# Performance work log

Measured on AMD Instinct MI355X. Metric: run time of the kernel, lower is better.

Reference implementation:

```python
import jax, jax.numpy as jnp
import numpy as np

D_MODEL = 2048
D_INNER = 2048
N_QK = 32
N_V = 32
D_STATE = 64
D_CONV = 4
CHUNK = 128
CONV_DIM = D_INNER + 2 * N_QK * D_STATE  # 6144
IN_OUT = 2 * D_INNER + 2 * N_QK * D_STATE + N_V  # 8224


def setup_inputs() -> dict:
    key = jax.random.key(0)
    ks = jax.random.split(key, 6)
    u = jax.random.normal(ks[0], (2, 4096, D_MODEL), dtype=jnp.float32)
    W_in = jax.random.normal(ks[1], (IN_OUT, D_MODEL), dtype=jnp.float32) * 0.02
    conv_w = jax.random.normal(ks[2], (CONV_DIM, D_CONV), dtype=jnp.float32) * 0.2
    conv_b = jax.random.normal(ks[3], (CONV_DIM,), dtype=jnp.float32) * 0.02
    D = jnp.ones((N_V,), dtype=jnp.float32)
    z_bias = jnp.zeros((D_INNER,), dtype=jnp.float32)
    W_out = jax.random.normal(ks[4], (D_MODEL, D_INNER), dtype=jnp.float32) * 0.02
    return {"u": u, "W_in": W_in, "conv_w": conv_w, "conv_b": conv_b,
            "D": D, "z_bias": z_bias, "W_out": W_out}


def causal_depthwise_conv(x, w, b):
    # x: [B, L, C]; w: [C, K]; b: [C]. Torch Conv1d(groups=C, padding=K-1)[..., :L]
    B, L, C = x.shape
    K = w.shape[1]
    xp = jnp.pad(x, ((0, 0), (K - 1, 0), (0, 0)))
    y = b[None, None, :]
    for k in range(K):
        y = y + xp[:, k:k + L, :] * w[None, None, :, k]
    return y


def ssd_chunk_scan(x, dt, B, C, chunk):
    # Mamba2 SSD with A = -1 per head.
    # x: [b,l,h,p], dt: [b,l,h] (positive), B,C: [b,l,h,n]
    b, l, h, p = x.shape
    n = B.shape[-1]
    nc = l // chunk
    x = x.reshape(b, nc, chunk, h, p)
    dt = dt.reshape(b, nc, chunk, h)
    B = B.reshape(b, nc, chunk, h, n)
    C = C.reshape(b, nc, chunk, h, n)
    a = -dt                                  # A * dt
    cum = jnp.cumsum(a, axis=2)              # [b,nc,q,h]
    xdt = x * dt[..., None]                  # dt_t * x_t
    # ---- intra-chunk (causal, decay exp(cum_q - cum_k), q >= k) ----
    CB = jnp.einsum('bcqhn,bckhn->bchqk', C, B)
    cumT = jnp.swapaxes(cum, 2, 3)           # [b,nc,h,q]
    diff = cumT[..., :, None] - cumT[..., None, :]   # [b,nc,h,q,k]
    mask = jnp.tril(jnp.ones((chunk, chunk), dtype=bool))
    decay = jnp.exp(jnp.where(mask, diff, -jnp.inf))
    y_intra = jnp.einsum('bchqk,bckhp->bcqhp', CB * decay, xdt)
    # ---- per-chunk final states ----
    state_decay = jnp.exp(cum[:, :, -1:, :] - cum)   # [b,nc,q,h]
    states = jnp.einsum('bckhn,bckhp->bchpn', B * state_decay[..., None], xdt)
    chunk_decay = jnp.exp(cum[:, :, -1, :])          # [b,nc,h]
    # ---- inter-chunk recurrence ----
    def step(carry, inp):
        st, cd = inp  # st [b,h,p,n], cd [b,h]
        new = carry * cd[:, :, None, None] + st
        return new, carry  # emit the state *entering* this chunk
    init = jnp.zeros((b, h, p, n), dtype=x.dtype)
    _, prev = jax.lax.scan(step, init,
                           (jnp.moveaxis(states, 1, 0), jnp.moveaxis(chunk_decay, 1, 0)))
    prev = jnp.moveaxis(prev, 0, 1)                  # [b,nc,h,p,n]
    y_inter = jnp.einsum('bcqhn,bchpn->bcqhp', C * jnp.exp(cum)[..., None], prev)
    return (y_intra + y_inter).reshape(b, l, h, p)


def reference(u, W_in, conv_w, conv_b, D, z_bias, W_out):
    b, l, _ = u.shape  # l divisible by CHUNK (padded_len == l)
    xBCzA = jnp.einsum('bld,od->blo', u, W_in)
    xBC = xBCzA[..., :CONV_DIM]
    z = xBCzA[..., CONV_DIM:CONV_DIM + D_INNER]
    A_log = xBCzA[..., CONV_DIM + D_INNER:]
    xBC = causal_depthwise_conv(xBC, conv_w, conv_b)  # activation = identity
    x = xBC[..., :D_INNER]
    Bm = xBC[..., D_INNER:D_INNER + N_QK * D_STATE]
    Cm = xBC[..., D_INNER + N_QK * D_STATE:]
    x = x.reshape(b, l, N_V, D_INNER // N_V)
    Bm = Bm.reshape(b, l, N_QK, D_STATE)
    Cm = Cm.reshape(b, l, N_QK, D_STATE)
    dt = jax.nn.softplus(A_log)                       # [b,l,h]
    x_scan = x / dt[..., None]
    y = ssd_chunk_scan(x_scan, dt, Bm, Cm, CHUNK)
    y = y + D[None, None, :, None] * x                # Du uses undivided x
    y = y.reshape(b, l, D_INNER)
    out = jnp.einsum('bli,oi->blo', y * jax.nn.silu(z + z_bias), W_out)
    return out
```

## Files before the change

kernel.cpp:

```cpp
#include <hip/hip_runtime.h>
#include <math.h>

#define D_MODEL  2048
#define D_INNER  2048
#define N_QK     32
#define N_V      32
#define D_STATE  64
#define D_CONV   4
#define CHUNK    128
#define CONV_DIM 6144
#define IN_OUT   8224
#define BATCH    2
#define SEQ      4096
#define M_ROWS   (BATCH*SEQ)
#define NCHUNK   (SEQ/CHUNK)

typedef unsigned short bf16_t;
typedef __attribute__((ext_vector_type(4))) float f32x4;
typedef __attribute__((ext_vector_type(8))) short bf16x8;

#define SWZ64(r,c)  ((((r)*64)  + (c)) ^ (((r)&7)<<3))
#define SWZ128(r,c) ((((r)*128) + (c)) ^ (((r)&7)<<3))

__device__ __forceinline__ float b2f(bf16_t u) {
    union { unsigned int i; float f; } w; w.i = ((unsigned int)u) << 16; return w.f;
}
__device__ __forceinline__ bf16_t f2b(float f) {
    unsigned int x = __float_as_uint(f);
    return (bf16_t)((x + 0x7FFFu + ((x >> 16) & 1u)) >> 16);
}
__device__ __forceinline__ void store4b(bf16_t* dst, float4 v) {
    ushort4 u; u.x = f2b(v.x); u.y = f2b(v.y); u.z = f2b(v.z); u.w = f2b(v.w);
    *reinterpret_cast<ushort4*>(dst) = u;
}

__device__ __forceinline__ void gload_lds16(const bf16_t* g, bf16_t* l) {
    __builtin_amdgcn_global_load_lds((const __attribute__((address_space(1))) void*)g,
                                     (__attribute__((address_space(3))) void*)l,
                                     16, 0, 0);
}

__global__ __launch_bounds__(256) void f2b3_kernel(const float* __restrict__ a0, bf16_t* __restrict__ o0, long n0,
                                                   const float* __restrict__ a1, bf16_t* __restrict__ o1, long n1,
                                                   const float* __restrict__ a2, bf16_t* __restrict__ o2, long n2)
{
    const long total = (n0 + n1 + n2) >> 2;
    for (long s = (long)blockIdx.x * 256 + threadIdx.x; s < total; s += (long)gridDim.x * 256) {
        long i = s << 2;
        const float* in; bf16_t* out;
        if (i < n0)           { in = a0 + i; out = o0 + i; }
        else if (i < n0 + n1) { i -= n0; in = a1 + i; out = o1 + i; }
        else                  { i -= n0 + n1; in = a2 + i; out = o2 + i; }
        float4 v = *reinterpret_cast<const float4*>(in);
        ushort4 o;
        o.x = f2b(v.x); o.y = f2b(v.y); o.z = f2b(v.z); o.w = f2b(v.w);
        *reinterpret_cast<ushort4*>(out) = o;
    }
}

template<int NTB, int K, bool OBF16>
__global__ __launch_bounds__(512, 2) void gemm256(const bf16_t* __restrict__ A,
                                                  const bf16_t* __restrict__ B,
                                                  void* __restrict__ Cv,
                                                  long ldc)
{
    constexpr int BK = 64;
    constexpr int NT = K / BK;
    __shared__ bf16_t As[2][2][8192];
    __shared__ bf16_t Bs[2][2][8192];

    const int nwg = gridDim.x;
    const int bid = blockIdx.x;
    const int wg  = ((nwg & 7) == 0) ? ((bid & 7) * (nwg >> 3) + (bid >> 3)) : bid;
    const int bm = (wg / NTB) * 256;
    const int bn = (wg % NTB) * 256;

    const int tid  = threadIdx.x;
    const int lane = tid & 63;
    const int wv   = tid >> 6;
    const int wr   = wv >> 2, wc = wv & 3;
    const int l15  = lane & 15, l4 = lane >> 4;

    f32x4 acc[8][4];
    #pragma unroll
    for (int i = 0; i < 8; ++i)
        #pragma unroll
        for (int j = 0; j < 4; ++j) acc[i][j] = (f32x4){0.f, 0.f, 0.f, 0.f};

    const bf16_t* Abase = A + (long)bm * K;
    const bf16_t* Bbase = B + (long)bn * K;

    auto stage_half = [&](int t, int buf, int kh) {
        #pragma unroll
        for (int it = 0; it < 2; ++it) {
            const int s   = it * 512 + tid;
            const int row = s >> 2;
            const int jp  = s & 3;
            const int jl  = jp ^ ((row >> 1) & 3);
            const long go = (long)row * K + t * BK + kh * 32 + jl * 8;
            gload_lds16(Abase + go, &As[buf][kh][s * 8]);
            gload_lds16(Bbase + go, &Bs[buf][kh][s * 8]);
        }
    };
    auto rdA = [&](int buf, int kh, int row) {
        const int jp = l4 ^ ((row >> 1) & 3);
        return *reinterpret_cast<const bf16x8*>(&As[buf][kh][(row * 4 + jp) * 8]);
    };
    auto rdB = [&](int buf, int kh, int row) {
        const int jp = l4 ^ ((row >> 1) & 3);
        return *reinterpret_cast<const bf16x8*>(&Bs[buf][kh][(row * 4 + jp) * 8]);
    };

    stage_half(0, 0, 0);
    stage_half(0, 0, 1);
    asm volatile("s_waitcnt vmcnt(4)" ::: "memory");
    __builtin_amdgcn_s_barrier();

    for (int t = 0; t < NT; ++t) {
        const int cur = t & 1;
        bf16x8 bfr[4], af[4];
        if (t + 1 < NT) stage_half(t + 1, cur ^ 1, 0);
        #pragma unroll
        for (int ni = 0; ni < 4; ++ni) bfr[ni] = rdB(cur, 0, wc * 64 + ni * 16 + l15);
        #pragma unroll
        for (int mi = 0; mi < 4; ++mi) af[mi] = rdA(cur, 0, wr * 128 + mi * 16 + l15);
        __builtin_amdgcn_s_setprio(1);
        #pragma unroll
        for (int mi = 0; mi < 4; ++mi)
            #pragma unroll
            for (int ni = 0; ni < 4; ++ni)
                acc[mi][ni] = __builtin_amdgcn_mfma_f32_16x16x32_bf16(
                    af[mi], bfr[ni], acc[mi][ni], 0, 0, 0);
        __builtin_amdgcn_s_setprio(0);
        #pragma unroll
        for (int mi = 0; mi < 4; ++mi) af[mi] = rdA(cur, 0, wr * 128 + 64 + mi * 16 + l15);
        __builtin_amdgcn_s_setprio(1);
        #pragma unroll
        for (int mi = 0; mi < 4; ++mi)
            #pragma unroll
            for (int ni = 0; ni < 4; ++ni)
                acc[4 + mi][ni] = __builtin_amdgcn_mfma_f32_16x16x32_bf16(
                    af[mi], bfr[ni], acc[4 + mi][ni], 0, 0, 0);
        __builtin_amdgcn_s_setprio(0);
        if (t + 1 < NT) {
            stage_half(t + 1, cur ^ 1, 1);
            asm volatile("s_waitcnt vmcnt(8)" ::: "memory");
        } else {
            asm volatile("s_waitcnt vmcnt(0)" ::: "memory");
        }
        __builtin_amdgcn_s_barrier();
        #pragma unroll
        for (int ni = 0; ni < 4; ++ni) bfr[ni] = rdB(cur, 1, wc * 64 + ni * 16 + l15);
        #pragma unroll
        for (int mi = 0; mi < 4; ++mi) af[mi] = rdA(cur, 1, wr * 128 + mi * 16 + l15);
        __builtin_amdgcn_s_setprio(1);
        #pragma unroll
        for (int mi = 0; mi < 4; ++mi)
            #pragma unroll
            for (int ni = 0; ni < 4; ++ni)
                acc[mi][ni] = __builtin_amdgcn_mfma_f32_16x16x32_bf16(
                    af[mi], bfr[ni], acc[mi][ni], 0, 0, 0);
        __builtin_amdgcn_s_setprio(0);
        #pragma unroll
        for (int mi = 0; mi < 4; ++mi) af[mi] = rdA(cur, 1, wr * 128 + 64 + mi * 16 + l15);
        __builtin_amdgcn_s_setprio(1);
        #pragma unroll
        for (int mi = 0; mi < 4; ++mi)
            #pragma unroll
            for (int ni = 0; ni < 4; ++ni)
                acc[4 + mi][ni] = __builtin_amdgcn_mfma_f32_16x16x32_bf16(
                    af[mi], bfr[ni], acc[4 + mi][ni], 0, 0, 0);
        __builtin_amdgcn_s_setprio(0);
        if (t + 1 < NT) { asm volatile("s_waitcnt vmcnt(4)" ::: "memory"); }
        __builtin_amdgcn_s_barrier();
    }

    #pragma unroll
    for (int mf = 0; mf < 8; ++mf) {
        const long grow0 = bm + wr * 128 + mf * 16 + l4 * 4;
        #pragma unroll
        for (int ni = 0; ni < 4; ++ni) {
            const int gcol = bn + wc * 64 + ni * 16 + l15;
            #pragma unroll
            for (int j = 0; j < 4; ++j) {
                if (OBF16)
                    ((bf16_t*)Cv)[(grow0 + j) * ldc + gcol] = f2b(acc[mf][ni][j]);
                else
                    ((float*)Cv)[(grow0 + j) * ldc + gcol] = acc[mf][ni][j];
            }
        }
    }
}

template<int N, int K, bool OBF16>
__global__ __launch_bounds__(256) void gemm_mfma(const bf16_t* __restrict__ A,
                                                 const bf16_t* __restrict__ B,
                                                 void* __restrict__ Cv,
                                                 long ldc)
{
    constexpr int BM = 128, BN = 128, BK = 64;
    constexpr int NTB = (N + BN - 1) / BN;
    __shared__ bf16_t As[BM * BK];
    __shared__ bf16_t Bs[BM * BK];

    const int nwg = gridDim.x;
    const int bid = blockIdx.x;
    const int wg  = ((nwg & 7) == 0) ? ((bid & 7) * (nwg >> 3) + (bid >> 3)) : bid;
    const int bm = (wg / NTB) * BM;
    const int bn = (wg % NTB) * BN;

    const int tid  = threadIdx.x;
    const int lane = tid & 63;
    const int wv   = tid >> 6;
    const int wr   = wv >> 1, wc = wv & 1;

    f32x4 acc[4][4];
    #pragma unroll
    for (int i = 0; i < 4; ++i)
        #pragma unroll
        for (int j = 0; j < 4; ++j) acc[i][j] = (f32x4){0.f, 0.f, 0.f, 0.f};

    for (int k0 = 0; k0 < K; k0 += BK) {
        #pragma unroll
        for (int it = 0; it < 4; ++it) {
            const int seg = it * 256 + tid;
            const int row = seg >> 3, c16 = seg & 7;
            gload_lds16(A + (long)(bm + row) * K + k0 + c16 * 8,
                        &As[row * BK + c16 * 8]);
            int brow = bn + row;
            if constexpr (N % BN != 0) brow = min(brow, N - 1);
            gload_lds16(B + (long)brow * K + k0 + c16 * 8,
                        &Bs[row * BK + c16 * 8]);
        }
        __syncthreads();
        #pragma unroll
        for (int kk = 0; kk < 2; ++kk) {
            bf16x8 af[4], bfr[4];
            const int kc = kk * 32 + (lane >> 4) * 8;
            #pragma unroll
            for (int mi = 0; mi < 4; ++mi) {
                const int row = wr * 64 + mi * 16 + (lane & 15);
                af[mi] = *reinterpret_cast<const bf16x8*>(&As[row * BK + kc]);
            }
            #pragma unroll
            for (int ni = 0; ni < 4; ++ni) {
                const int row = wc * 64 + ni * 16 + (lane & 15);
                bfr[ni] = *reinterpret_cast<const bf16x8*>(&Bs[row * BK + kc]);
            }
            #pragma unroll
            for (int mi = 0; mi < 4; ++mi)
                #pragma unroll
                for (int ni = 0; ni < 4; ++ni)
                    acc[mi][ni] = __builtin_amdgcn_mfma_f32_16x16x32_bf16(
                        af[mi], bfr[ni], acc[mi][ni], 0, 0, 0);
        }
        __syncthreads();
    }

    #pragma unroll
    for (int mi = 0; mi < 4; ++mi) {
        const long row0 = bm + wr * 64 + mi * 16 + ((lane >> 4) << 2);
        #pragma unroll
        for (int ni = 0; ni < 4; ++ni) {
            const int col = bn + wc * 64 + ni * 16 + (lane & 15);
            if (N % BN != 0 && col >= N) continue;
            #pragma unroll
            for (int j = 0; j < 4; ++j) {
                if (OBF16)
                    ((bf16_t*)Cv)[(row0 + j) * ldc + col] = f2b(acc[mi][ni][j]);
                else
                    ((float*)Cv)[(row0 + j) * ldc + col] = acc[mi][ni][j];
            }
        }
    }
}

__device__ __forceinline__ float4 conv4v(const bf16_t* __restrict__ xb, long m, int l,
                                         int col, const float* __restrict__ cw,
                                         const float* __restrict__ cbv)
{
    float4 acc = *reinterpret_cast<const float4*>(cbv + col);
    float4 wc0 = *reinterpret_cast<const float4*>(cw + (long)col * 4);
    float4 wc1 = *reinterpret_cast<const float4*>(cw + (long)col * 4 + 4);
    float4 wc2 = *reinterpret_cast<const float4*>(cw + (long)col * 4 + 8);
    float4 wc3 = *reinterpret_cast<const float4*>(cw + (long)col * 4 + 12);
    const float t0[4] = {wc0.x, wc0.y, wc0.z, wc0.w};
    const float t1[4] = {wc1.x, wc1.y, wc1.z, wc1.w};
    const float t2[4] = {wc2.x, wc2.y, wc2.z, wc2.w};
    const float t3[4] = {wc3.x, wc3.y, wc3.z, wc3.w};
    #pragma unroll
    for (int tap = 0; tap < 4; ++tap) {
        if (l - 3 + tap < 0) continue;
        const bf16_t* p = xb + (m - 3 + tap) * (long)IN_OUT + col;
        ushort4 v = *reinterpret_cast<const ushort4*>(p);
        acc.x = fmaf(b2f(v.x), t0[tap], acc.x);
        acc.y = fmaf(b2f(v.y), t1[tap], acc.y);
        acc.z = fmaf(b2f(v.z), t2[tap], acc.z);
        acc.w = fmaf(b2f(v.w), t3[tap], acc.w);
    }
    return acc;
}

template<bool EXP>
__global__ __launch_bounds__(512, 4) void ssd_states(const bf16_t* __restrict__ xb,
                                                     const float* __restrict__ cw,
                                                     const float* __restrict__ cbv,
                                                     bf16_t* __restrict__ states,
                                                     float* __restrict__ cumbuf,
                                                     float* __restrict__ cdecay,
                                                     bf16_t* __restrict__ xtg,
                                                     bf16_t* __restrict__ bg)
{
    const int h = blockIdx.x, c = blockIdx.y, b = blockIdx.z;
    __shared__ bf16_t sx [128 * 64];
    __shared__ bf16_t sBr[128 * 64];
    __shared__ bf16_t sXT[64 * 128];
    __shared__ bf16_t sBT[64 * 128];
    __shared__ float  cum[CHUNK];
    __shared__ float  w0tot;
    const int t = threadIdx.x;
    const long mbase = (long)b * SEQ + (long)c * CHUNK;
    const long cb = ((long)b * NCHUNK + c) * N_QK + h;

    float v = 0.f;
    if (t < CHUNK) {
        const float a = b2f(xb[(mbase + t) * (long)IN_OUT + (CONV_DIM + D_INNER) + h]);
        v = -((a > 20.f) ? a : log1pf(expf(a)));
        #pragma unroll
        for (int s = 1; s < 64; s <<= 1) {
            const float u2 = __shfl_up(v, s, 64);
            if ((t & 63) >= s) v += u2;
        }
        if (t == 63) w0tot = v;
    }
    for (int idx = t; idx < CHUNK * 16; idx += 512) {
        const int k = idx >> 4, q4 = (idx & 15) * 4;
        const long m = mbase + k;
        const int l = (int)(m & (SEQ - 1));
        float4 xv = conv4v(xb, m, l, h * 64 + q4, cw, cbv);
        float4 bv = conv4v(xb, m, l, D_INNER + h * 64 + q4, cw, cbv);
        store4b(&sx [SWZ64(k, q4)], xv);
        store4b(&sBr[SWZ64(k, q4)], bv);
    }
    __syncthreads();
    if (t >= 64 && t < CHUNK) v += w0tot;
    if (t < CHUNK) cum[t] = v;
    __syncthreads();
    const float clast = cum[CHUNK - 1];
    {
        const int j = t & 127;
        const int c8b = (t >> 7) * 2;
        const float ej = __expf(clast - cum[j]);
        #pragma unroll
        for (int it = 0; it < 2; ++it) {
            const int c8 = c8b + it;
            bf16x8 xv = *reinterpret_cast<const bf16x8*>(&sx [SWZ64(j, c8 * 8)]);
            bf16x8 bv = *reinterpret_cast<const bf16x8*>(&sBr[SWZ64(j, c8 * 8)]);
            #pragma unroll
            for (int e = 0; e < 8; ++e) {
                sXT[SWZ128(c8 * 8 + e, j)] = xv[e];
                sBT[SWZ128(c8 * 8 + e, j)] = f2b(b2f((bf16_t)bv[e]) * ej);
            }
        }
    }
    __syncthreads();

    const int lane = t & 63, wv = t >> 6;
    const int l15 = lane & 15, l4 = lane >> 4;
    const int prow  = (wv & 3) * 16;
    const int nbase = (wv >> 2) * 2;
    f32x4 acc[2];
    acc[0] = (f32x4){0.f, 0.f, 0.f, 0.f};
    acc[1] = (f32x4){0.f, 0.f, 0.f, 0.f};
    #pragma unroll
    for (int ks = 0; ks < 4; ++ks) {
        const int kc = ks * 32 + l4 * 8;
        bf16x8 af = *reinterpret_cast<const bf16x8*>(&sXT[SWZ128(prow + l15, kc)]);
        #pragma unroll
        for (int nj = 0; nj < 2; ++nj) {
            bf16x8 bf = *reinterpret_cast<const bf16x8*>(&sBT[SWZ128((nbase + nj) * 16 + l15, kc)]);
            acc[nj] = __builtin_amdgcn_mfma_f32_16x16x32_bf16(af, bf, acc[nj], 0, 0, 0);
        }
    }
    #pragma unroll
    for (int nj = 0; nj < 2; ++nj) {
        #pragma unroll
        for (int jj = 0; jj < 4; ++jj) {
            const int p = prow + l4 * 4 + jj;
            states[cb * 4096 + SWZ64(p, (nbase + nj) * 16 + l15)] = f2b(acc[nj][jj]);
        }
    }
    if constexpr (EXP) {
        #pragma unroll
        for (int it = 0; it < 2; ++it) {
            const int s = it * 512 + t;
            *reinterpret_cast<bf16x8*>(xtg + cb * 8192 + s * 8) =
                *reinterpret_cast<const bf16x8*>(&sXT[s * 8]);
            *reinterpret_cast<bf16x8*>(bg + cb * 8192 + s * 8) =
                *reinterpret_cast<const bf16x8*>(&sBr[s * 8]);
        }
    }
    if (t < CHUNK) cumbuf[cb * CHUNK + t] = cum[t];
    if (t == 0)   cdecay[cb] = __expf(clast);
}

__global__ __launch_bounds__(256) void ssd_scan(bf16_t* __restrict__ states,
                                                const float* __restrict__ cdecay)
{
    const int bid = blockIdx.x;
    const int bh = bid >> 2, q = bid & 3;
    const int b = bh >> 5, h = bh & 31;
    const int t = threadIdx.x;
    __shared__ bf16_t sst[NCHUNK * 1024];
    __shared__ float  scd[NCHUNK];
    if (t < NCHUNK) scd[t] = cdecay[((long)b * NCHUNK + t) * N_QK + h];
    #pragma unroll
    for (int it = 0; it < 16; ++it) {
        const int slot = it * 256 + t;
        const int c = slot >> 7, off = (slot & 127) * 8;
        const long g = (((long)b * NCHUNK + c) * N_QK + h) * 4096 + q * 1024 + off;
        gload_lds16(states + g, &sst[slot * 8]);
    }
    __syncthreads();
    float4 carry = make_float4(0.f, 0.f, 0.f, 0.f);
    for (int c = 0; c < NCHUNK; ++c) {
        ushort4* p = reinterpret_cast<ushort4*>(&sst[c * 1024 + t * 4]);
        const ushort4 su = *p;
        ushort4 pv;
        pv.x = f2b(carry.x); pv.y = f2b(carry.y);
        pv.z = f2b(carry.z); pv.w = f2b(carry.w);
        *p = pv;
        const float cd = scd[c];
        carry.x = fmaf(carry.x, cd, b2f(su.x));
        carry.y = fmaf(carry.y, cd, b2f(su.y));
        carry.z = fmaf(carry.z, cd, b2f(su.z));
        carry.w = fmaf(carry.w, cd, b2f(su.w));
    }
    __syncthreads();
    #pragma unroll
    for (int it = 0; it < 16; ++it) {
        const int slot = it * 256 + t;
        const int c = slot >> 7, off = (slot & 127) * 8;
        const long g = (((long)b * NCHUNK + c) * N_QK + h) * 4096 + q * 1024 + off;
        *reinterpret_cast<bf16x8*>(states + g) =
            *reinterpret_cast<const bf16x8*>(&sst[slot * 8]);
    }
}

template<bool EXP>
__global__ __launch_bounds__(512, 4) void ssd_out(const bf16_t* __restrict__ xb,
                                                  const float* __restrict__ cumbuf,
                                                  const bf16_t* __restrict__ prevst,
                                                  const float* __restrict__ Dvec,
                                                  const float* __restrict__ zbias,
                                                  const float* __restrict__ cw,
                                                  const float* __restrict__ cbv,
                                                  const bf16_t* __restrict__ xtg,
                                                  const bf16_t* __restrict__ bg,
                                                  bf16_t* __restrict__ yz)
{
    const int h = blockIdx.x, c = blockIdx.y, b = blockIdx.z;
    __shared__ bf16_t sC[128 * 64];
    __shared__ bf16_t sB[128 * 64];
    __shared__ bf16_t sXQ[128 * 64];
    __shared__ bf16_t sXT[64 * 128];
    __shared__ bf16_t sP[64 * 64];
    __shared__ float  cum[CHUNK];
    const int t = threadIdx.x;
    const long mbase = (long)b * SEQ + (long)c * CHUNK;
    const long cb = ((long)b * NCHUNK + c) * N_QK + h;
    if (t < CHUNK) cum[t] = cumbuf[cb * CHUNK + t];
    gload_lds16(prevst + cb * 4096 + t * 8, &sP[t * 8]);
    if constexpr (EXP) {
        #pragma unroll
        for (int it = 0; it < 2; ++it) {
            const int s = it * 512 + t;
            gload_lds16(bg  + cb * 8192 + s * 8, &sB [s * 8]);
            gload_lds16(xtg + cb * 8192 + s * 8, &sXT[s * 8]);
        }
        for (int idx = t; idx < CHUNK * 16; idx += 512) {
            const int k = idx >> 4, q4 = (idx & 15) * 4;
            const long m = mbase + k;
            const int l = (int)(m & (SEQ - 1));
            float4 cv = conv4v(xb, m, l, 2 * D_INNER + h * 64 + q4, cw, cbv);
            store4b(&sC[SWZ64(k, q4)], cv);
        }
        __syncthreads();
    } else {
        for (int idx = t; idx < CHUNK * 16; idx += 512) {
            const int k = idx >> 4, q4 = (idx & 15) * 4;
            const long m = mbase + k;
            const int l = (int)(m & (SEQ - 1));
            float4 xv = conv4v(xb, m, l, h * 64 + q4, cw, cbv);
            float4 bv = conv4v(xb, m, l, D_INNER + h * 64 + q4, cw, cbv);
            float4 cv = conv4v(xb, m, l, 2 * D_INNER + h * 64 + q4, cw, cbv);
            store4b(&sXQ[SWZ64(k, q4)], xv);
            store4b(&sB [SWZ64(k, q4)], bv);
            store4b(&sC [SWZ64(k, q4)], cv);
        }
        __syncthreads();
        {
            const int j = t & 127;
            const int c8b = (t >> 7) * 2;
            #pragma unroll
            for (int it = 0; it < 2; ++it) {
                const int c8 = c8b + it;
                bf16x8 v = *reinterpret_cast<const bf16x8*>(&sXQ[SWZ64(j, c8 * 8)]);
                #pragma unroll
                for (int e = 0; e < 8; ++e) sXT[SWZ128(c8 * 8 + e, j)] = v[e];
            }
        }
        __syncthreads();
    }

    const int lane = t & 63, wv = t >> 6;
    const int w16 = wv * 16, l15 = lane & 15, l4 = lane >> 4;
    bf16_t* sQ = sXQ;

    f32x4 yac[4], iac[4];
    #pragma unroll
    for (int np = 0; np < 4; ++np) {
        yac[np] = (f32x4){0.f, 0.f, 0.f, 0.f};
        iac[np] = (f32x4){0.f, 0.f, 0.f, 0.f};
    }

    #pragma unroll
    for (int H = 0; H < 2; ++H) {
        if (H == 1 && wv < 4) break;
        const int j0 = H * 64;
        f32x4 sac[4];
        #pragma unroll
        for (int nj = 0; nj < 4; ++nj) sac[nj] = (f32x4){0.f, 0.f, 0.f, 0.f};
        #pragma unroll
        for (int kk = 0; kk < 2; ++kk) {
            const int kc = kk * 32 + l4 * 8;
            bf16x8 af0 = *reinterpret_cast<const bf16x8*>(&sC[SWZ64(w16 + l15, kc)]);
            #pragma unroll
            for (int nj = 0; nj < 4; ++nj) {
                if (j0 + nj * 16 <= w16 + 15) {
                    bf16x8 bfj = *reinterpret_cast<const bf16x8*>(&sB[SWZ64(j0 + nj * 16 + l15, kc)]);
                    sac[nj] = __builtin_amdgcn_mfma_f32_16x16x32_bf16(af0, bfj, sac[nj], 0, 0, 0);
                }
            }
        }
        #pragma unroll
        for (int nj = 0; nj < 4; ++nj) {
            const int jcol = nj * 16 + l15;
            const int jg = j0 + jcol;
            #pragma unroll
            for (int jj = 0; jj < 4; ++jj) {
                const int i = w16 + l4 * 4 + jj;
                const float q = (jg <= i) ? __expf(cum[i] - cum[jg]) * sac[nj][jj] : 0.f;
                sQ[SWZ64(i, jcol)] = f2b(q);
            }
        }
        #pragma unroll
        for (int kk = 0; kk < 2; ++kk) {
            const int kc = kk * 32 + l4 * 8;
            bf16x8 qa = *reinterpret_cast<const bf16x8*>(&sQ[SWZ64(w16 + l15, kc)]);
            #pragma unroll
            for (int np = 0; np < 4; ++np) {
                bf16x8 xf = *reinterpret_cast<const bf16x8*>(&sXT[SWZ128(np * 16 + l15, j0 + kc)]);
                yac[np] = __builtin_amdgcn_mfma_f32_16x16x32_bf16(qa, xf, yac[np], 0, 0, 0);
            }
        }
    }
    #pragma unroll
    for (int kk = 0; kk < 2; ++kk) {
        const int kc = kk * 32 + l4 * 8;
        bf16x8 cf = *reinterpret_cast<const bf16x8*>(&sC[SWZ64(w16 + l15, kc)]);
        #pragma unroll
        for (int np = 0; np < 4; ++np) {
            bf16x8 pf = *reinterpret_cast<const bf16x8*>(&sP[SWZ64(np * 16 + l15, kc)]);
            iac[np] = __builtin_amdgcn_mfma_f32_16x16x32_bf16(cf, pf, iac[np], 0, 0, 0);
        }
    }
    const float dh = Dvec[h];
    #pragma unroll
    for (int jj = 0; jj < 4; ++jj) {
        const int i = w16 + l4 * 4 + jj;
        const float ei = __expf(cum[i]);
        const long m = mbase + i;
        const bf16_t* zr = xb + m * (long)IN_OUT + CONV_DIM + h * 64;
        bf16_t* orow = yz + m * (long)D_INNER + h * 64;
        #pragma unroll
        for (int np = 0; np < 4; ++np) {
            const int p = np * 16 + l15;
            const float xval = b2f(sXT[SWZ128(p, i)]);
            const float y = yac[np][jj] + ei * iac[np][jj] + dh * xval;
            const float zv = b2f(zr[p]) + zbias[h * 64 + p];
            const float s = zv / (1.f + __expf(-zv));
            orow[p] = f2b(y * s);
        }
    }
}

extern "C" void kernel_launch(void* const* d_in, const int* in_sizes, int n_in,
                              void* d_out, int out_size, void* d_ws, size_t ws_size,
                              hipStream_t stream)
{
    const float* u      = (const float*)d_in[0];
    const float* W_in   = (const float*)d_in[1];
    const float* conv_w = (const float*)d_in[2];
    const float* conv_b = (const float*)d_in[3];
    const float* Dv     = (const float*)d_in[4];
    const float* z_bias = (const float*)d_in[5];
    const float* W_out  = (const float*)d_in[6];
    float* out = (float*)d_out;

    char* w = (char*)d_ws;
    bf16_t* xbcza = (bf16_t*)w;  w += (long)M_ROWS * IN_OUT * 2;
    bf16_t* wob   = (bf16_t*)w;  w += (long)2048 * 2048 * 2;
    char* ureg = w;  w += 67239936;
    bf16_t* ub  = (bf16_t*)ureg;
    bf16_t* wib = (bf16_t*)(ureg + (long)M_ROWS * D_MODEL * 2);
    bf16_t* yzb = (bf16_t*)ureg;
    float*  cumb   = (float*)(ureg + (long)M_ROWS * D_INNER * 2);
    bf16_t* states = (bf16_t*)(cumb + (long)BATCH * NCHUNK * N_QK * CHUNK);
    float*  cdec   = (float*)(states + (long)BATCH * NCHUNK * N_QK * 4096);
    const long base_bytes = (long)(w - (char*)d_ws);
    const long exp_bytes  = 2L * 2048 * 8192 * 2;
    const bool use_exp = ((long)ws_size >= base_bytes + exp_bytes);
    bf16_t* xtg = (bf16_t*)w;
    bf16_t* bg  = xtg + (long)2048 * 8192;

    {
        const long n0 = (long)M_ROWS * D_MODEL;
        const long n1 = (long)IN_OUT * D_MODEL;
        const long n2 = (long)D_MODEL * D_INNER;
        f2b3_kernel<<<2048, 256, 0, stream>>>(u, ub, n0, W_in, wib, n1, W_out, wob, n2);
    }

    gemm256<32, D_MODEL, true><<<(M_ROWS / 256) * 32, 512, 0, stream>>>(
        ub, wib, xbcza, IN_OUT);
    gemm_mfma<32, D_MODEL, true><<<(M_ROWS / 128), 256, 0, stream>>>(
        ub, wib + (long)8192 * D_MODEL, xbcza + 8192, IN_OUT);

    if (use_exp) {
        ssd_states<true><<<dim3(N_QK, NCHUNK, BATCH), 512, 0, stream>>>(
            xbcza, conv_w, conv_b, states, cumb, cdec, xtg, bg);
        ssd_scan<<<BATCH * N_QK * 4, 256, 0, stream>>>(states, cdec);
        ssd_out<true><<<dim3(N_QK, NCHUNK, BATCH), 512, 0, stream>>>(
            xbcza, cumb, states, Dv, z_bias, conv_w, conv_b, xtg, bg, yzb);
    } else {
        ssd_states<false><<<dim3(N_QK, NCHUNK, BATCH), 512, 0, stream>>>(
            xbcza, conv_w, conv_b, states, cumb, cdec, nullptr, nullptr);
        ssd_scan<<<BATCH * N_QK * 4, 256, 0, stream>>>(states, cdec);
        ssd_out<false><<<dim3(N_QK, NCHUNK, BATCH), 512, 0, stream>>>(
            xbcza, cumb, states, Dv, z_bias, conv_w, conv_b, nullptr, nullptr, yzb);
    }

    gemm256<8, D_INNER, false><<<(M_ROWS / 256) * 8, 512, 0, stream>>>(
        yzb, wob, out, D_MODEL);
}
```

Measured before the change: 730.8 us.

## Split-K the narrow A_log projection, precompute softplus dt, widen scan grid

The 32-column A_log projection used to run as a 128x128-tile GEMM on only 64 workgroups, with most of each B tile padding. It is replaced by a split-K kernel over 256 workgroups with a 32-wide B tile and swizzled LDS. A small reduction kernel sums the four partials and applies softplus into an fp32 dt buffer, which ssd_states now reads directly. The chunk-state scan is also split 8 ways per head instead of 4, doubling its grid and halving per-thread work. The cost is one extra launch and extra global traffic for the partial sums, placed in reused workspace.

Result: faster. 713.1 us (-2.4%).

```diff
diff --git a/kernel.cpp b/kernel.cpp
--- a/kernel.cpp
+++ b/kernel.cpp
@@ -192,86 +192,76 @@
     }
 }
 
-template<int N, int K, bool OBF16>
-__global__ __launch_bounds__(256) void gemm_mfma(const bf16_t* __restrict__ A,
-                                                 const bf16_t* __restrict__ B,
-                                                 void* __restrict__ Cv,
-                                                 long ldc)
-{
-    constexpr int BM = 128, BN = 128, BK = 64;
-    constexpr int NTB = (N + BN - 1) / BN;
-    __shared__ bf16_t As[BM * BK];
-    __shared__ bf16_t Bs[BM * BK];
-
-    const int nwg = gridDim.x;
-    const int bid = blockIdx.x;
-    const int wg  = ((nwg & 7) == 0) ? ((bid & 7) * (nwg >> 3) + (bid >> 3)) : bid;
-    const int bm = (wg / NTB) * BM;
-    const int bn = (wg % NTB) * BN;
-
-    const int tid  = threadIdx.x;
-    const int lane = tid & 63;
-    const int wv   = tid >> 6;
-    const int wr   = wv >> 1, wc = wv & 1;
-
-    f32x4 acc[4][4];
-    #pragma unroll
-    for (int i = 0; i < 4; ++i)
-        #pragma unroll
-        for (int j = 0; j < 4; ++j) acc[i][j] = (f32x4){0.f, 0.f, 0.f, 0.f};
-
-    for (int k0 = 0; k0 < K; k0 += BK) {
+__global__ __launch_bounds__(256) void alog_partial(const bf16_t* __restrict__ A,
+                                                    const bf16_t* __restrict__ Bt,
+                                                    float* __restrict__ P)
+{
+    const int rb = blockIdx.x & 63, ks = blockIdx.x >> 6;
+    const int bm = rb * 128;
+    __shared__ bf16_t As[128 * 64];
+    __shared__ bf16_t Bs[32 * 64];
+    const int tid = threadIdx.x, lane = tid & 63, wv = tid >> 6;
+    const int l15 = lane & 15, l4 = lane >> 4;
+
+    f32x4 acc[2][2];
+    #pragma unroll
+    for (int mi = 0; mi < 2; ++mi)
+        #pragma unroll
+        for (int nj = 0; nj < 2; ++nj) acc[mi][nj] = (f32x4){0.f, 0.f, 0.f, 0.f};
+
+    for (int it8 = 0; it8 < 8; ++it8) {
+        const long kbase = (long)ks * 512 + it8 * 64;
         #pragma unroll
         for (int it = 0; it < 4; ++it) {
-            const int seg = it * 256 + tid;
-            const int row = seg >> 3, c16 = seg & 7;
-            gload_lds16(A + (long)(bm + row) * K + k0 + c16 * 8,
-                        &As[row * BK + c16 * 8]);
-            int brow = bn + row;
-            if constexpr (N % BN != 0) brow = min(brow, N - 1);
-            gload_lds16(B + (long)brow * K + k0 + c16 * 8,
-                        &Bs[row * BK + c16 * 8]);
+            const int s = it * 256 + tid;
+            const int row = s >> 3, c16 = s & 7;
+            gload_lds16(A + (long)(bm + row) * D_MODEL + kbase + (c16 ^ (row & 7)) * 8,
+                        &As[s * 8]);
+        }
+        {
+            const int row = tid >> 3, c16 = tid & 7;
+            gload_lds16(Bt + (long)row * D_MODEL + kbase + (c16 ^ (row & 7)) * 8,
+                        &Bs[tid * 8]);
         }
         __syncthreads();
         #pragma unroll
         for (int kk = 0; kk < 2; ++kk) {
-            bf16x8 af[4], bfr[4];
-            const int kc = kk * 32 + (lane >> 4) * 8;
-            #pragma unroll
-            for (int mi = 0; mi < 4; ++mi) {
-                const int row = wr * 64 + mi * 16 + (lane & 15);
-                af[mi] = *reinterpret_cast<const bf16x8*>(&As[row * BK + kc]);
-            }
-            #pragma unroll
-            for (int ni = 0; ni < 4; ++ni) {
-                const int row = wc * 64 + ni * 16 + (lane & 15);
-                bfr[ni] = *reinterpret_cast<const bf16x8*>(&Bs[row * BK + kc]);
-            }
-            #pragma unroll
-            for (int mi = 0; mi < 4; ++mi)
+            bf16x8 bf[2], af;
+            #pragma unroll
+            for (int nj = 0; nj < 2; ++nj) {
+                const int row = nj * 16 + l15;
+                bf[nj] = *reinterpret_cast<const bf16x8*>(&Bs[row * 64 + (((kk * 4 + l4) ^ (row & 7)) << 3)]);
+            }
+            #pragma unroll
+            for (int mi = 0; mi < 2; ++mi) {
+                const int row = wv * 32 + mi * 16 + l15;
+                af = *reinterpret_cast<const bf16x8*>(&As[row * 64 + (((kk * 4 + l4) ^ (row & 7)) << 3)]);
                 #pragma unroll
-                for (int ni = 0; ni < 4; ++ni)
-                    acc[mi][ni] = __builtin_amdgcn_mfma_f32_16x16x32_bf16(
-                        af[mi], bfr[ni], acc[mi][ni], 0, 0, 0);
+                for (int nj = 0; nj < 2; ++nj)
+                    acc[mi][nj] = __builtin_amdgcn_mfma_f32_16x16x32_bf16(af, bf[nj], acc[mi][nj], 0, 0, 0);
+            }
         }
         __syncthreads();
     }
-
-    #pragma unroll
-    for (int mi = 0; mi < 4; ++mi) {
-        const long row0 = bm + wr * 64 + mi * 16 + ((lane >> 4) << 2);
-        #pragma unroll
-        for (int ni = 0; ni < 4; ++ni) {
-            const int col = bn + wc * 64 + ni * 16 + (lane & 15);
-            if (N % BN != 0 && col >= N) continue;
+    #pragma unroll
+    for (int mi = 0; mi < 2; ++mi)
+        #pragma unroll
+        for (int nj = 0; nj < 2; ++nj)
             #pragma unroll
             for (int j = 0; j < 4; ++j) {
-                if (OBF16)
-                    ((bf16_t*)Cv)[(row0 + j) * ldc + col] = f2b(acc[mi][ni][j]);
-                else
-                    ((float*)Cv)[(row0 + j) * ldc + col] = acc[mi][ni][j];
-            }
-        }
+                const int row = bm + wv * 32 + mi * 16 + l4 * 4 + j;
+                P[(long)ks * (M_ROWS * 32) + (long)row * 32 + nj * 16 + l15] = acc[mi][nj][j];
+            }
+}
+
+__global__ __launch_bounds__(256) void alog_fin(const float* __restrict__ P,
+                                                float* __restrict__ dt)
+{
+    const long i = (long)blockIdx.x * 256 + threadIdx.x;
+    if (i < (long)M_ROWS * 32) {
+        const long n = (long)M_ROWS * 32;
+        const float a = P[i] + P[n + i] + P[2 * n + i] + P[3 * n + i];
+        dt[i] = (a > 20.f) ? a : log1pf(expf(a));
     }
 }
 
@@ -303,6 +293,7 @@
 
 template<bool EXP>
 __global__ __launch_bounds__(512, 4) void ssd_states(const bf16_t* __restrict__ xb,
+                                                     const float* __restrict__ dtb,
                                                      const float* __restrict__ cw,
                                                      const float* __restrict__ cbv,
                                                      bf16_t* __restrict__ states,
@@ -324,8 +315,7 @@
 
     float v = 0.f;
     if (t < CHUNK) {
-        const float a = b2f(xb[(mbase + t) * (long)IN_OUT + (CONV_DIM + D_INNER) + h]);
-        v = -((a > 20.f) ? a : log1pf(expf(a)));
+        v = -dtb[(mbase + t) * N_V + h];
         #pragma unroll
         for (int s = 1; s < 64; s <<= 1) {
             const float u2 = __shfl_up(v, s, 64);
@@ -408,40 +398,37 @@
                                                 const float* __restrict__ cdecay)
 {
     const int bid = blockIdx.x;
-    const int bh = bid >> 2, q = bid & 3;
+    const int bh = bid >> 3, q = bid & 7;
     const int b = bh >> 5, h = bh & 31;
     const int t = threadIdx.x;
-    __shared__ bf16_t sst[NCHUNK * 1024];
+    __shared__ bf16_t sst[NCHUNK * 512];
     __shared__ float  scd[NCHUNK];
     if (t < NCHUNK) scd[t] = cdecay[((long)b * NCHUNK + t) * N_QK + h];
     #pragma unroll
-    for (int it = 0; it < 16; ++it) {
+    for (int it = 0; it < 8; ++it) {
         const int slot = it * 256 + t;
-        const int c = slot >> 7, off = (slot & 127) * 8;
-        const long g = (((long)b * NCHUNK + c) * N_QK + h) * 4096 + q * 1024 + off;
+        const int c = slot >> 6, off = (slot & 63) * 8;
+        const long g = (((long)b * NCHUNK + c) * N_QK + h) * 4096 + q * 512 + off;
         gload_lds16(states + g, &sst[slot * 8]);
     }
     __syncthreads();
-    float4 carry = make_float4(0.f, 0.f, 0.f, 0.f);
+    float2 carry = make_float2(0.f, 0.f);
     for (int c = 0; c < NCHUNK; ++c) {
-        ushort4* p = reinterpret_cast<ushort4*>(&sst[c * 1024 + t * 4]);
-        const ushort4 su = *p;
-        ushort4 pv;
+        ushort2* p = reinterpret_cast<ushort2*>(&sst[c * 512 + t * 2]);
+        const ushort2 su = *p;
+        ushort2 pv;
         pv.x = f2b(carry.x); pv.y = f2b(carry.y);
-        pv.z = f2b(carry.z); pv.w = f2b(carry.w);
         *p = pv;
         const float cd = scd[c];
         carry.x = fmaf(carry.x, cd, b2f(su.x));
         carry.y = fmaf(carry.y, cd, b2f(su.y));
-        carry.z = fmaf(carry.z, cd, b2f(su.z));
-        carry.w = fmaf(carry.w, cd, b2f(su.w));
     }
     __syncthreads();
     #pragma unroll
-    for (int it = 0; it < 16; ++it) {
+    for (int it = 0; it < 8; ++it) {
         const int slot = it * 256 + t;
-        const int c = slot >> 7, off = (slot & 127) * 8;
-        const long g = (((long)b * NCHUNK + c) * N_QK + h) * 4096 + q * 1024 + off;
+        const int c = slot >> 6, off = (slot & 63) * 8;
+        const long g = (((long)b * NCHUNK + c) * N_QK + h) * 4096 + q * 512 + off;
         *reinterpret_cast<bf16x8*>(states + g) =
             *reinterpret_cast<const bf16x8*>(&sst[slot * 8]);
     }
@@ -618,6 +605,8 @@
     float*  cumb   = (float*)(ureg + (long)M_ROWS * D_INNER * 2);
     bf16_t* states = (bf16_t*)(cumb + (long)BATCH * NCHUNK * N_QK * CHUNK);
     float*  cdec   = (float*)(states + (long)BATCH * NCHUNK * N_QK * 4096);
+    float* partials = (float*)(ureg + 50331648);
+    float* dtb      = (float*)(ureg + 54525952);
     const long base_bytes = (long)(w - (char*)d_ws);
     const long exp_bytes  = 2L * 2048 * 8192 * 2;
     const bool use_exp = ((long)ws_size >= base_bytes + exp_bytes);
@@ -633,19 +622,20 @@
 
     gemm256<32, D_MODEL, true><<<(M_ROWS / 256) * 32, 512, 0, stream>>>(
         ub, wib, xbcza, IN_OUT);
-    gemm_mfma<32, D_MODEL, true><<<(M_ROWS / 128), 256, 0, stream>>>(
-        ub, wib + (long)8192 * D_MODEL, xbcza + 8192, IN_OUT);
+
+    alog_partial<<<256, 256, 0, stream>>>(ub, wib + (long)8192 * D_MODEL, partials);
+    alog_fin<<<(M_ROWS * 32 + 255) / 256, 256, 0, stream>>>(partials, dtb);
 
     if (use_exp) {
         ssd_states<true><<<dim3(N_QK, NCHUNK, BATCH), 512, 0, stream>>>(
-            xbcza, conv_w, conv_b, states, cumb, cdec, xtg, bg);
-        ssd_scan<<<BATCH * N_QK * 4, 256, 0, stream>>>(states, cdec);
+            xbcza, dtb, conv_w, conv_b, states, cumb, cdec, xtg, bg);
+        ssd_scan<<<BATCH * N_QK * 8, 256, 0, stream>>>(states, cdec);
         ssd_out<true><<<dim3(N_QK, NCHUNK, BATCH), 512, 0, stream>>>(
             xbcza, cumb, states, Dv, z_bias, conv_w, conv_b, xtg, bg, yzb);
     } else {
         ssd_states<false><<<dim3(N_QK, NCHUNK, BATCH), 512, 0, stream>>>(
-            xbcza, conv_w, conv_b, states, cumb, cdec, nullptr, nullptr);
-        ssd_scan<<<BATCH * N_QK * 4, 256, 0, stream>>>(states, cdec);
+            xbcza, dtb, conv_w, conv_b, states, cumb, cdec, nullptr, nullptr);
+        ssd_scan<<<BATCH * N_QK * 8, 256, 0, stream>>>(states, cdec);
         ssd_out<false><<<dim3(N_QK, NCHUNK, BATCH), 512, 0, stream>>>(
             xbcza, cumb, states, Dv, z_bias, conv_w, conv_b, nullptr, nullptr, yzb);
     }
```
